# Kernel tuning notes

Hardware: AMD Instinct MI355X
Metric: run time of the kernel (lower is better)

Reference implementation:

```python
import jax, jax.numpy as jnp
import numpy as np

N_LAYERS = 4
D_MODEL = 64        # 8*8 hardcoded in source
D_STATE = 128
D_CONV = 4
EXPAND = 2
HEADDIM = 64        # Mamba2Simple default
D_INNER = EXPAND * D_MODEL            # 128
NHEADS = D_INNER // HEADDIM           # 2
NGROUPS = 1
D_IN_PROJ = 2 * D_INNER + 2 * NGROUPS * D_STATE + NHEADS   # 514
CONV_DIM = D_INNER + 2 * NGROUPS * D_STATE                 # 384
EPS = 1e-5
B_SZ, SEQ = 8, 4096


def setup_inputs() -> dict:
    key = jax.random.key(0)
    ks = jax.random.split(key, 8)
    s = 0.02
    x = jax.random.normal(ks[0], (B_SZ, SEQ, D_MODEL), jnp.float32)
    in_proj_w = jax.random.normal(ks[1], (N_LAYERS, D_IN_PROJ, D_MODEL), jnp.float32) * s
    conv_w = jax.random.normal(ks[2], (N_LAYERS, CONV_DIM, 1, D_CONV), jnp.float32) * 0.2
    conv_b = jnp.zeros((N_LAYERS, CONV_DIM), jnp.float32)
    # dt_bias ~ inverse-softplus of small dt values
    dt_bias = jax.random.uniform(ks[3], (N_LAYERS, NHEADS), jnp.float32, -4.0, 0.0)
    A_log = jnp.log(jax.random.uniform(ks[4], (N_LAYERS, NHEADS), jnp.float32, 1.0, 16.0))
    D = jnp.ones((N_LAYERS, NHEADS), jnp.float32)
    norm_w = jnp.ones((N_LAYERS, D_INNER), jnp.float32)
    out_proj_w = jax.random.normal(ks[5], (N_LAYERS, D_MODEL, D_INNER), jnp.float32) * s
    return {"x": x, "in_proj_w": in_proj_w, "conv_w": conv_w, "conv_b": conv_b,
            "dt_bias": dt_bias, "A_log": A_log, "D": D, "norm_w": norm_w,
            "out_proj_w": out_proj_w}


def _ssm(xh, dt, A, Bm, Cm):
    """Selective-scan SSM. xh:(B,L,H,P) dt:(B,L,H) A:(H,) Bm,Cm:(B,L,S) -> (B,L,H,P)"""
    dA = jnp.exp(dt * A)  # (B,L,H)

    def step(h, inp):
        dA_t, dt_t, x_t, B_t, C_t = inp
        # h: (B,H,P,S)
        h = h * dA_t[:, :, None, None] + (dt_t[:, :, None] * x_t)[..., None] * B_t[:, None, None, :]
        y = jnp.einsum('bhps,bs->bhp', h, C_t)
        return h, y

    b = xh.shape[0]
    h0 = jnp.zeros((b, NHEADS, HEADDIM, D_STATE), xh.dtype)
    xs = (jnp.moveaxis(dA, 1, 0), jnp.moveaxis(dt, 1, 0), jnp.moveaxis(xh, 1, 0),
          jnp.moveaxis(Bm, 1, 0), jnp.moveaxis(Cm, 1, 0))
    _, ys = jax.lax.scan(step, h0, xs)
    return jnp.moveaxis(ys, 0, 1)


def _layer(x, p):
    in_w, cw, cb, dtb, Alog, Dp, nw, ow = p
    zxbcdt = x @ in_w.T                                   # (B,L,514)
    z = zxbcdt[..., :D_INNER]
    xBC = zxbcdt[..., D_INNER:D_INNER + CONV_DIM]
    dt = jax.nn.softplus(zxbcdt[..., -NHEADS:] + dtb)     # (B,L,H)
    # causal depthwise conv over sequence
    xc = jnp.moveaxis(xBC, -1, 1)                         # (B,C,L)
    xc = jax.lax.conv_general_dilated(xc, cw, (1,), [(D_CONV - 1, 0)],
                                      dimension_numbers=('NCH', 'OIH', 'NCH'),
                                      feature_group_count=CONV_DIM)
    xBC = jax.nn.silu(jnp.moveaxis(xc + cb[None, :, None], 1, -1))
    xs = xBC[..., :D_INNER]
    Bm = xBC[..., D_INNER:D_INNER + D_STATE]
    Cm = xBC[..., D_INNER + D_STATE:]
    xh = xs.reshape(xs.shape[0], xs.shape[1], NHEADS, HEADDIM)
    A = -jnp.exp(Alog)                                    # (H,)
    y = _ssm(xh, dt, A, Bm, Cm) + Dp[None, None, :, None] * xh
    y = y.reshape(y.shape[0], y.shape[1], D_INNER)
    # gated RMSNorm (norm_before_gate=False): rmsnorm(y * silu(z)) * w
    y = y * jax.nn.silu(z)
    y = y * jax.lax.rsqrt(jnp.mean(y * y, axis=-1, keepdims=True) + EPS) * nw
    return y @ ow.T


def reference(x, in_proj_w, conv_w, conv_b, dt_bias, A_log, D, norm_w, out_proj_w):
    def body(xc, p):
        return _layer(xc, p) + xc, None
    out, _ = jax.lax.scan(body, x, (in_proj_w, conv_w, conv_b, dt_bias, A_log, D, norm_w, out_proj_w))
    return out
```

## Files before the change

kernel.cpp:

```cpp
#include <hip/hip_runtime.h>
#include <math.h>

#define B_SZ 8
#define SEQ  4096
#define DM   64
#define DI   128
#define NH   2
#define HD   64
#define DS   128
#define DIP  514
#define ZW   512
#define CD   384
#define QC   64
#define NC   64
#define NR   (B_SZ*SEQ)
#define WPAD 576

typedef __attribute__((ext_vector_type(8))) short bf16x8;
typedef __attribute__((ext_vector_type(4))) float f32x4;

__device__ __forceinline__ unsigned short f2bf(float f) {
    union { float f; unsigned int u; } x; x.f = f;
    unsigned int r = x.u + 0x7fffu + ((x.u >> 16) & 1u);
    return (unsigned short)(r >> 16);
}
__device__ __forceinline__ float bf2f(unsigned short h) {
    union { unsigned int u; float f; } x; x.u = ((unsigned int)h) << 16;
    return x.f;
}
__device__ __forceinline__ bf16x8 fragld(const unsigned short* base, int r0, int k0, int ld) {
    int l = threadIdx.x & 63;
    return *(const bf16x8*)(base + (size_t)(r0 + (l & 15)) * ld + k0 + (l >> 4) * 8);
}

__global__ __launch_bounds__(256) void k_wcvt(const float* __restrict__ in_w,
                                              const float* __restrict__ out_w,
                                              unsigned short* __restrict__ Wb,
                                              unsigned short* __restrict__ OWb) {
    int idx = blockIdx.x * 256 + threadIdx.x;
    if (idx < 4 * WPAD * 64) {
        int l = idx / (WPAD * 64), r = idx % (WPAD * 64);
        int n = r >> 6, k = r & 63;
        float v = (n < DIP) ? in_w[(size_t)l * DIP * 64 + (size_t)n * 64 + k] : 0.f;
        Wb[idx] = f2bf(v);
    }
    if (idx < 4 * 64 * 128) OWb[idx] = f2bf(out_w[idx]);
}

__global__ __launch_bounds__(256) void k_xcvt(const float* __restrict__ X,
                                              unsigned short* __restrict__ Xb) {
    int idx = (blockIdx.x * 256 + threadIdx.x) * 4;
    float4 v = *(const float4*)(X + idx);
    uint2 p;
    p.x = f2bf(v.x) | ((unsigned int)f2bf(v.y) << 16);
    p.y = f2bf(v.z) | ((unsigned int)f2bf(v.w) << 16);
    *(uint2*)(Xb + idx) = p;
}

__global__ __launch_bounds__(256) void k_inproj(const unsigned short* __restrict__ Xb,
                                                const unsigned short* __restrict__ Wb,
                                                unsigned short* __restrict__ ZXb,
                                                float* __restrict__ DT) {
    int m0 = blockIdx.x * 256;
    int n0 = blockIdx.y * 64;
    int tid = threadIdx.x;
    int wid = tid >> 6, lane = tid & 63;
    int q4 = lane >> 4, c16 = lane & 15;
    int mb = m0 + wid * 64;
    bf16x8 af[4][2];
#pragma unroll
    for (int mt = 0; mt < 4; mt++)
#pragma unroll
        for (int ks = 0; ks < 2; ks++)
            af[mt][ks] = *(const bf16x8*)(Xb + (size_t)(mb + mt * 16 + c16) * 64 + ks * 32 + q4 * 8);
    if (n0 < 512) {
#pragma unroll
        for (int nt = 0; nt < 4; nt++) {
            bf16x8 bf[2];
#pragma unroll
            for (int ks = 0; ks < 2; ks++)
                bf[ks] = *(const bf16x8*)(Wb + (size_t)(n0 + nt * 16 + c16) * 64 + ks * 32 + q4 * 8);
#pragma unroll
            for (int mt = 0; mt < 4; mt++) {
                f32x4 acc = {0.f, 0.f, 0.f, 0.f};
                acc = __builtin_amdgcn_mfma_f32_16x16x32_bf16(af[mt][0], bf[0], acc, 0, 0, 0);
                acc = __builtin_amdgcn_mfma_f32_16x16x32_bf16(af[mt][1], bf[1], acc, 0, 0, 0);
#pragma unroll
                for (int rr = 0; rr < 4; rr++) {
                    float v = acc[rr];
                    float vn = __shfl_xor(v, 1);
                    if (!(lane & 1)) {
                        unsigned int pk = f2bf(v) | ((unsigned int)f2bf(vn) << 16);
                        *(unsigned int*)(ZXb + (size_t)(mb + mt * 16 + q4 * 4 + rr) * ZW + n0 + nt * 16 + c16) = pk;
                    }
                }
            }
        }
    } else {
        bf16x8 bf[2];
#pragma unroll
        for (int ks = 0; ks < 2; ks++)
            bf[ks] = *(const bf16x8*)(Wb + (size_t)(512 + c16) * 64 + ks * 32 + q4 * 8);
#pragma unroll
        for (int mt = 0; mt < 4; mt++) {
            f32x4 acc = {0.f, 0.f, 0.f, 0.f};
            acc = __builtin_amdgcn_mfma_f32_16x16x32_bf16(af[mt][0], bf[0], acc, 0, 0, 0);
            acc = __builtin_amdgcn_mfma_f32_16x16x32_bf16(af[mt][1], bf[1], acc, 0, 0, 0);
            if (c16 < 2)
#pragma unroll
                for (int rr = 0; rr < 4; rr++)
                    DT[(size_t)(mb + mt * 16 + q4 * 4 + rr) * 2 + c16] = acc[rr];
        }
    }
}

__global__ __launch_bounds__(512, 4) void k_chunk1(
        const unsigned short* __restrict__ ZXb, const float* __restrict__ DT,
        const float* __restrict__ CW, const float* __restrict__ CB,
        const float* __restrict__ dtb, const float* __restrict__ Alog,
        const float* __restrict__ Dv,
        unsigned short* __restrict__ SL, unsigned short* __restrict__ CBuf,
        float* __restrict__ EB,
        float* __restrict__ TB, unsigned short* __restrict__ YBb) {
    __shared__ unsigned short sBt[128][72];
    __shared__ unsigned short sXt[128][72];
    __shared__ unsigned short uBC[2][64][136];
    __shared__ float s_cum[2][64], s_dt[2][64], s_w[2][64];
    unsigned short (*sM)[64][72] = (unsigned short (*)[64][72])&uBC[0][0][0];

    int c = blockIdx.x, b = blockIdx.y;
    size_t rbase = (size_t)b * SEQ + c * QC;
    int tid = threadIdx.x;
    int wid = tid >> 6, lane = tid & 63;

    if (wid < 2) {
        int h = wid, j = lane;
        float raw = DT[(rbase + j) * 2 + h] + dtb[h];
        float dt = (raw > 20.f) ? raw : log1pf(__expf(raw));
        float A = -__expf(Alog[h]);
        float x = dt * A;
        for (int off = 1; off < 64; off <<= 1) {
            float o = __shfl_up(x, off);
            if (lane >= off) x += o;
        }
        float T = __shfl(x, 63);
        s_dt[h][j] = dt;
        s_cum[h][j] = x;
        s_w[h][j] = __expf(T - x) * dt;
        EB[((size_t)(b * NC + c)) * 128 + h * 64 + j] = __expf(x);
        if (j == 0) TB[(b * 2 + h) * NC + c] = __expf(T);
    }
    __syncthreads();

    size_t cbbase = ((size_t)(b * NC + c)) * 8192;
    for (int e = tid; e < 64 * 96; e += 512) {
        int j = e / 96;
        int q = e - j * 96;
        int cc = q * 4;
        int l = c * QC + j;
        const unsigned short* zp = ZXb + (rbase + j) * ZW + 128 + cc;
        uint2 a0 = *(const uint2*)zp;
        uint2 a1 = make_uint2(0, 0), a2 = make_uint2(0, 0), a3 = make_uint2(0, 0);
        if (l >= 1) a1 = *(const uint2*)(zp - ZW);
        if (l >= 2) a2 = *(const uint2*)(zp - 2 * ZW);
        if (l >= 3) a3 = *(const uint2*)(zp - 3 * ZW);
        float v[4];
#pragma unroll
        for (int u = 0; u < 4; u++) {
            unsigned int w0 = (u < 2) ? a0.x : a0.y;
            unsigned int w1 = (u < 2) ? a1.x : a1.y;
            unsigned int w2 = (u < 2) ? a2.x : a2.y;
            unsigned int w3 = (u < 2) ? a3.x : a3.y;
            int sh = (u & 1) * 16;
            float r0 = bf2f((unsigned short)(w0 >> sh));
            float r1 = bf2f((unsigned short)(w1 >> sh));
            float r2 = bf2f((unsigned short)(w2 >> sh));
            float r3 = bf2f((unsigned short)(w3 >> sh));
            float4 wv = *(const float4*)(CW + (cc + u) * 4);
            float t = CB[cc + u] + wv.w * r0 + wv.z * r1 + wv.y * r2 + wv.x * r3;
            v[u] = t / (1.f + __expf(-t));
        }
        if (cc < 128) {
#pragma unroll
            for (int u = 0; u < 4; u++) sXt[cc + u][j] = f2bf(v[u]);
        } else if (cc < 256) {
            int s = cc - 128;
            unsigned int p0 = f2bf(v[0]) | ((unsigned int)f2bf(v[1]) << 16);
            unsigned int p1 = f2bf(v[2]) | ((unsigned int)f2bf(v[3]) << 16);
            *(uint2*)&uBC[0][j][s] = make_uint2(p0, p1);
#pragma unroll
            for (int u = 0; u < 4; u++) sBt[s + u][j] = f2bf(v[u]);
        } else {
            int s = cc - 256;
            unsigned int p0 = f2bf(v[0]) | ((unsigned int)f2bf(v[1]) << 16);
            unsigned int p1 = f2bf(v[2]) | ((unsigned int)f2bf(v[3]) << 16);
            *(uint2*)&uBC[1][j][s] = make_uint2(p0, p1);
            *(uint2*)(CBuf + cbbase + (size_t)j * 128 + s) = make_uint2(p0, p1);
        }
    }
    __syncthreads();

    int q4 = lane >> 4, c16 = lane & 15;
    f32x4 gacc[2];
#pragma unroll
    for (int u = 0; u < 2; u++) {
        int t = wid * 2 + u;
        int it = t >> 2, jt = t & 3;
        f32x4 acc = {0.f, 0.f, 0.f, 0.f};
        for (int ks = 0; ks < 4; ks++) {
            bf16x8 a = fragld(&uBC[1][0][0], it * 16, ks * 32, 136);
            bf16x8 bb = fragld(&uBC[0][0][0], jt * 16, ks * 32, 136);
            acc = __builtin_amdgcn_mfma_f32_16x16x32_bf16(a, bb, acc, 0, 0, 0);
        }
        gacc[u] = acc;
    }
    __syncthreads();
#pragma unroll
    for (int u = 0; u < 2; u++) {
        int t = wid * 2 + u;
        int it = t >> 2, jt = t & 3;
        int j = jt * 16 + c16;
        for (int rr = 0; rr < 4; rr++) {
            int i = it * 16 + q4 * 4 + rr;
            float gv = gacc[u][rr];
            for (int h = 0; h < 2; h++) {
                float m = 0.f;
                if (j <= i) m = gv * __expf(s_cum[h][i] - s_cum[h][j]) * s_dt[h][j];
                sM[h][i][j] = f2bf(m);
            }
        }
    }
    __syncthreads();

#pragma unroll
    for (int u = 0; u < 4; u++) {
        int idx = wid * 4 + u;
        int h = idx >> 4, tt = idx & 15;
        int it = tt >> 2, pt = tt & 3;
        float dco = Dv[h];
        int pg = h * 64 + pt * 16 + c16;
        f32x4 acc;
        for (int rr = 0; rr < 4; rr++) {
            int i = it * 16 + q4 * 4 + rr;
            acc[rr] = dco * bf2f(sXt[pg][i]);
        }
        for (int ks = 0; ks < 2; ks++) {
            bf16x8 a = fragld(&sM[h][0][0], it * 16, ks * 32, 72);
            bf16x8 bb = fragld(&sXt[0][0], h * 64 + pt * 16, ks * 32, 72);
            acc = __builtin_amdgcn_mfma_f32_16x16x32_bf16(a, bb, acc, 0, 0, 0);
        }
        for (int rr = 0; rr < 4; rr++) {
            int i = it * 16 + q4 * 4 + rr;
            float v = acc[rr];
            float vn = __shfl_xor(v, 1);
            if (!(lane & 1)) {
                unsigned int pk = f2bf(v) | ((unsigned int)f2bf(vn) << 16);
                *(unsigned int*)(YBb + (rbase + i) * DI + pg) = pk;
            }
        }
    }
    size_t slbase = ((size_t)(b * NC + c)) * 16384;
#pragma unroll
    for (int u = 0; u < 8; u++) {
        int idx = wid * 8 + u;
        int ptl = idx >> 3, st = idx & 7;
        int h = ptl >> 2;
        f32x4 acc = {0.f, 0.f, 0.f, 0.f};
        for (int ks = 0; ks < 2; ks++) {
            int jb = ks * 32 + (lane >> 4) * 8;
            bf16x8 a = fragld(&sXt[0][0], ptl * 16, ks * 32, 72);
            bf16x8 aw;
#pragma unroll
            for (int t = 0; t < 8; t++) aw[t] = (short)f2bf(bf2f((unsigned short)a[t]) * s_w[h][jb + t]);
            bf16x8 bb = fragld(&sBt[0][0], st * 16, ks * 32, 72);
            acc = __builtin_amdgcn_mfma_f32_16x16x32_bf16(aw, bb, acc, 0, 0, 0);
        }
        int s = st * 16 + c16;
        for (int rr = 0; rr < 4; rr++) {
            int p = ptl * 16 + q4 * 4 + rr;
            float vv = acc[rr];
            float vn = __shfl_xor(vv, 1);
            if (!(lane & 1)) {
                unsigned int pk = f2bf(vv) | ((unsigned int)f2bf(vn) << 16);
                *(unsigned int*)(SL + slbase + (size_t)p * 128 + s) = pk;
            }
        }
    }
}

__global__ __launch_bounds__(256) void k_scan(unsigned short* __restrict__ SL,
                                              const float* __restrict__ TB) {
    int bid = blockIdx.x;
    int b = bid >> 6;
    int ps = (bid & 63) * 256 + threadIdx.x;
    int h = ps >> 13;
    const float* dAp = TB + (b * 2 + h) * NC;
    size_t base = (size_t)(b * NC) * 16384 + ps;
    float hacc = 0.f;
#pragma unroll 8
    for (int cc = 0; cc < NC; cc++) {
        size_t idx = base + (size_t)cc * 16384;
        float slv = bf2f(SL[idx]);
        SL[idx] = f2bf(hacc);
        hacc = hacc * dAp[cc] + slv;
    }
}

__global__ __launch_bounds__(512, 2) void k_fused(
        const unsigned short* __restrict__ SL, const unsigned short* __restrict__ CBuf,
        const float* __restrict__ EB,
        const unsigned short* __restrict__ YBb, const unsigned short* __restrict__ ZXb,
        const float* __restrict__ NW, const unsigned short* __restrict__ OWb,
        unsigned short* __restrict__ Xb, float* __restrict__ OutF, int last) {
    __shared__ __attribute__((aligned(16))) unsigned short sH[128][136];
    __shared__ __attribute__((aligned(16))) unsigned short sE[128][136];
    float* sGf = (float*)&sH[0][0];
    unsigned short (*sG)[136] = (unsigned short (*)[136])&sE[0][0];

    int c = blockIdx.x, b = blockIdx.y;
    size_t rbase = (size_t)b * SEQ + c * QC;
    int tid = threadIdx.x;
    int wid = tid >> 6, lane = tid & 63;
    size_t base = ((size_t)(b * NC + c)) * 16384;
    for (int u = 0; u < 4; u++) {
        int e = u * 512 + tid;
        int row = e >> 4, cb8 = (e & 15) * 8;
        *(uint4*)&sH[row][cb8] = *(const uint4*)(SL + base + (size_t)row * 128 + cb8);
    }
    size_t cbbase = ((size_t)(b * NC + c)) * 8192;
    size_t ebase  = ((size_t)(b * NC + c)) * 128;
    for (int u = 0; u < 2; u++) {
        int idx8 = u * 512 + tid;
        int i = idx8 >> 4, sc = (idx8 & 15) * 8;
        uint4 cv = *(const uint4*)(CBuf + cbbase + (size_t)i * 128 + sc);
        float e0 = EB[ebase + i], e1 = EB[ebase + 64 + i];
        unsigned int w[4] = {cv.x, cv.y, cv.z, cv.w};
        uint4 o0, o1;
        unsigned int* po0 = &o0.x;
        unsigned int* po1 = &o1.x;
#pragma unroll
        for (int t = 0; t < 4; t++) {
            float lo = bf2f((unsigned short)(w[t] & 0xffff));
            float hi = bf2f((unsigned short)(w[t] >> 16));
            po0[t] = f2bf(lo * e0) | ((unsigned int)f2bf(hi * e0) << 16);
            po1[t] = f2bf(lo * e1) | ((unsigned int)f2bf(hi * e1) << 16);
        }
        *(uint4*)&sE[i][sc] = o0;
        *(uint4*)&sE[64 + i][sc] = o1;
    }
    __syncthreads();
    int q4 = lane >> 4, c16 = lane & 15;

    float yv[4][4];
    int tit[4], tpg[4];
#pragma unroll
    for (int u = 0; u < 4; u++) {
        int idx = wid * 4 + u;
        int h = idx >> 4, tt = idx & 15;
        int it = tt >> 2, pt = tt & 3;
        f32x4 acc = {0.f, 0.f, 0.f, 0.f};
        for (int ks = 0; ks < 4; ks++) {
            bf16x8 a = fragld(&sE[0][0], h * 64 + it * 16, ks * 32, 136);
            bf16x8 bb = fragld(&sH[0][0], h * 64 + pt * 16, ks * 32, 136);
            acc = __builtin_amdgcn_mfma_f32_16x16x32_bf16(a, bb, acc, 0, 0, 0);
        }
        int pg = h * 64 + pt * 16 + c16;
        tit[u] = it; tpg[u] = pg;
        for (int rr = 0; rr < 4; rr++) {
            int i = it * 16 + q4 * 4 + rr;
            float y = acc[rr] + bf2f(YBb[(rbase + i) * DI + pg]);
            float z = bf2f(ZXb[(rbase + i) * ZW + pg]);
            yv[u][rr] = y * (z / (1.f + __expf(-z)));
        }
    }
    __syncthreads();
#pragma unroll
    for (int u = 0; u < 4; u++)
        for (int rr = 0; rr < 4; rr++) {
            int i = tit[u] * 16 + q4 * 4 + rr;
            sGf[i * 132 + tpg[u]] = yv[u][rr];
        }
    __syncthreads();
    {
        int row = tid >> 3, p0 = (tid & 7) * 16;
        float g[16];
        float ss = 0.f;
        for (int t2 = 0; t2 < 16; t2++) { g[t2] = sGf[row * 132 + p0 + t2]; ss += g[t2] * g[t2]; }
        ss += __shfl_xor(ss, 1);
        ss += __shfl_xor(ss, 2);
        ss += __shfl_xor(ss, 4);
        float rms = rsqrtf(ss * (1.f / 128.f) + 1e-5f);
        for (int t2 = 0; t2 < 16; t2 += 2) {
            unsigned int pk = f2bf(g[t2] * rms * NW[p0 + t2]) |
                              ((unsigned int)f2bf(g[t2 + 1] * rms * NW[p0 + t2 + 1]) << 16);
            *(unsigned int*)&sG[row][p0 + t2] = pk;
        }
    }
    __syncthreads();
#pragma unroll
    for (int u = 0; u < 2; u++) {
        int t = wid * 2 + u;
        int mt = t >> 2, nt = t & 3;
        f32x4 acc = {0.f, 0.f, 0.f, 0.f};
        for (int ks = 0; ks < 4; ks++) {
            bf16x8 a = fragld(&sG[0][0], mt * 16, ks * 32, 136);
            bf16x8 bb = *(const bf16x8*)(OWb + (size_t)(nt * 16 + c16) * 128 + ks * 32 + q4 * 8);
            acc = __builtin_amdgcn_mfma_f32_16x16x32_bf16(a, bb, acc, 0, 0, 0);
        }
        for (int rr = 0; rr < 4; rr++) {
            int m = mt * 16 + q4 * 4 + rr;
            int n = nt * 16 + c16;
            size_t o = (rbase + m) * DM + n;
            float v = bf2f(Xb[o]) + acc[rr];
            if (last) {
                OutF[o] = v;
            } else {
                float vn = __shfl_xor(v, 1);
                if (!(lane & 1)) {
                    unsigned int pk = f2bf(v) | ((unsigned int)f2bf(vn) << 16);
                    *(unsigned int*)(Xb + o) = pk;
                }
            }
        }
    }
}

extern "C" void kernel_launch(void* const* d_in, const int* in_sizes, int n_in,
                              void* d_out, int out_size, void* d_ws, size_t ws_size,
                              hipStream_t stream) {
    const float* x       = (const float*)d_in[0];
    const float* in_w    = (const float*)d_in[1];
    const float* conv_w  = (const float*)d_in[2];
    const float* conv_b  = (const float*)d_in[3];
    const float* dt_bias = (const float*)d_in[4];
    const float* A_log   = (const float*)d_in[5];
    const float* Dp      = (const float*)d_in[6];
    const float* norm_w  = (const float*)d_in[7];
    const float* out_w   = (const float*)d_in[8];
    float* out = (float*)d_out;
    float* ws  = (float*)d_ws;

    float* dt = ws;
    float* tb = dt + (size_t)NR * 2;
    float* eb = tb + 1024;
    unsigned short* zxb  = (unsigned short*)(eb + (size_t)B_SZ * NC * 128);
    unsigned short* ybb  = zxb + (size_t)NR * ZW;
    unsigned short* sl   = ybb + (size_t)NR * DI;
    unsigned short* cbuf = sl + (size_t)B_SZ * NC * 16384;
    unsigned short* xb   = cbuf + (size_t)B_SZ * NC * 8192;
    unsigned short* wb   = xb + (size_t)NR * DM;
    unsigned short* owb  = wb + (size_t)4 * WPAD * 64;

    k_wcvt<<<(4 * WPAD * 64 + 255) / 256, 256, 0, stream>>>(in_w, out_w, wb, owb);
    k_xcvt<<<NR * DM / 1024, 256, 0, stream>>>(x, xb);

    for (int layer = 0; layer < 4; layer++) {
        k_inproj<<<dim3(NR / 256, 9), 256, 0, stream>>>(xb, wb + (size_t)layer * WPAD * 64, zxb, dt);
        k_chunk1<<<dim3(NC, B_SZ), 512, 0, stream>>>(zxb, dt,
                conv_w + (size_t)layer * CD * 4, conv_b + (size_t)layer * CD,
                dt_bias + layer * NH, A_log + layer * NH, Dp + layer * NH,
                sl, cbuf, eb, tb, ybb);
        k_scan<<<512, 256, 0, stream>>>(sl, tb);
        k_fused<<<dim3(NC, B_SZ), 512, 0, stream>>>(sl, cbuf, eb, ybb, zxb,
                norm_w + layer * DI, owb + (size_t)layer * 64 * 128, xb, out,
                (layer == 3) ? 1 : 0);
    }
}
```

Baseline: 370.3 us.

## Fuse in-projection GEMM into chunk kernel, keep xBC and dt in shared memory

Removes the separate in-projection kernel and computes the projection per chunk inside the chunk kernel, now run with 1024 threads. Only the z part goes to global memory, narrowed to 128 columns. The xBC columns, plus a 3-row halo recomputed from the previous chunk for the causal conv, stay in shared memory, and dt stays in shared memory too. This cuts the global write and read-back of the 512-wide bf16 projection buffer and the dt buffer, and saves one launch per layer. In exchange the halo rows are recomputed, shared memory use grows, and the 1024-thread blocks may lower occupancy.

Result: slower. 414.2 us (+11.9%).

```diff
diff --git a/kernel.cpp b/kernel.cpp
--- a/kernel.cpp
+++ b/kernel.cpp
@@ -9,12 +9,12 @@
 #define HD   64
 #define DS   128
 #define DIP  514
-#define ZW   512
 #define CD   384
 #define QC   64
 #define NC   64
 #define NR   (B_SZ*SEQ)
 #define WPAD 576
+#define ZLD  388
 
 typedef __attribute__((ext_vector_type(8))) short bf16x8;
 typedef __attribute__((ext_vector_type(4))) float f32x4;
@@ -30,7 +30,7 @@
 }
 __device__ __forceinline__ bf16x8 fragld(const unsigned short* base, int r0, int k0, int ld) {
     int l = threadIdx.x & 63;
-    return *(const bf16x8*)(base + (size_t)(r0 + (l & 15)) * ld + k0 + (l >> 4) * 8);
+    return *(const bf16x8*)(base + (ptrdiff_t)(r0 + (l & 15)) * ld + k0 + (l >> 4) * 8);
 }
 
 __global__ __launch_bounds__(256) void k_wcvt(const float* __restrict__ in_w,
@@ -57,85 +57,77 @@
     *(uint2*)(Xb + idx) = p;
 }
 
-__global__ __launch_bounds__(256) void k_inproj(const unsigned short* __restrict__ Xb,
-                                                const unsigned short* __restrict__ Wb,
-                                                unsigned short* __restrict__ ZXb,
-                                                float* __restrict__ DT) {
-    int m0 = blockIdx.x * 256;
-    int n0 = blockIdx.y * 64;
-    int tid = threadIdx.x;
-    int wid = tid >> 6, lane = tid & 63;
-    int q4 = lane >> 4, c16 = lane & 15;
-    int mb = m0 + wid * 64;
-    bf16x8 af[4][2];
-#pragma unroll
-    for (int mt = 0; mt < 4; mt++)
-#pragma unroll
-        for (int ks = 0; ks < 2; ks++)
-            af[mt][ks] = *(const bf16x8*)(Xb + (size_t)(mb + mt * 16 + c16) * 64 + ks * 32 + q4 * 8);
-    if (n0 < 512) {
-#pragma unroll
-        for (int nt = 0; nt < 4; nt++) {
-            bf16x8 bf[2];
-#pragma unroll
-            for (int ks = 0; ks < 2; ks++)
-                bf[ks] = *(const bf16x8*)(Wb + (size_t)(n0 + nt * 16 + c16) * 64 + ks * 32 + q4 * 8);
-#pragma unroll
-            for (int mt = 0; mt < 4; mt++) {
-                f32x4 acc = {0.f, 0.f, 0.f, 0.f};
-                acc = __builtin_amdgcn_mfma_f32_16x16x32_bf16(af[mt][0], bf[0], acc, 0, 0, 0);
-                acc = __builtin_amdgcn_mfma_f32_16x16x32_bf16(af[mt][1], bf[1], acc, 0, 0, 0);
-#pragma unroll
-                for (int rr = 0; rr < 4; rr++) {
-                    float v = acc[rr];
-                    float vn = __shfl_xor(v, 1);
-                    if (!(lane & 1)) {
-                        unsigned int pk = f2bf(v) | ((unsigned int)f2bf(vn) << 16);
-                        *(unsigned int*)(ZXb + (size_t)(mb + mt * 16 + q4 * 4 + rr) * ZW + n0 + nt * 16 + c16) = pk;
-                    }
-                }
-            }
-        }
-    } else {
-        bf16x8 bf[2];
-#pragma unroll
-        for (int ks = 0; ks < 2; ks++)
-            bf[ks] = *(const bf16x8*)(Wb + (size_t)(512 + c16) * 64 + ks * 32 + q4 * 8);
-#pragma unroll
-        for (int mt = 0; mt < 4; mt++) {
-            f32x4 acc = {0.f, 0.f, 0.f, 0.f};
-            acc = __builtin_amdgcn_mfma_f32_16x16x32_bf16(af[mt][0], bf[0], acc, 0, 0, 0);
-            acc = __builtin_amdgcn_mfma_f32_16x16x32_bf16(af[mt][1], bf[1], acc, 0, 0, 0);
-            if (c16 < 2)
-#pragma unroll
-                for (int rr = 0; rr < 4; rr++)
-                    DT[(size_t)(mb + mt * 16 + q4 * 4 + rr) * 2 + c16] = acc[rr];
-        }
-    }
-}
-
-__global__ __launch_bounds__(512, 4) void k_chunk1(
-        const unsigned short* __restrict__ ZXb, const float* __restrict__ DT,
+__global__ __launch_bounds__(1024) void k_mega(
+        const unsigned short* __restrict__ Xb, const unsigned short* __restrict__ Wb,
         const float* __restrict__ CW, const float* __restrict__ CB,
         const float* __restrict__ dtb, const float* __restrict__ Alog,
         const float* __restrict__ Dv,
+        unsigned short* __restrict__ Zb,
         unsigned short* __restrict__ SL, unsigned short* __restrict__ CBuf,
         float* __restrict__ EB,
         float* __restrict__ TB, unsigned short* __restrict__ YBb) {
+    __shared__ unsigned short zrc[68 * ZLD];
     __shared__ unsigned short sBt[128][72];
     __shared__ unsigned short sXt[128][72];
     __shared__ unsigned short uBC[2][64][136];
-    __shared__ float s_cum[2][64], s_dt[2][64], s_w[2][64];
+    __shared__ float s_cum[2][64], s_dt[2][64], s_w[2][64], s_dtraw[2][64];
     unsigned short (*sM)[64][72] = (unsigned short (*)[64][72])&uBC[0][0][0];
 
     int c = blockIdx.x, b = blockIdx.y;
     size_t rbase = (size_t)b * SEQ + c * QC;
     int tid = threadIdx.x;
     int wid = tid >> 6, lane = tid & 63;
+    int q4 = lane >> 4, c16 = lane & 15;
+
+    for (int t = wid; t < 156; t += 16) {
+        int row0, col0, mode, mt, zc0 = 0;
+        if (t < 32) {
+            mt = t >> 3; col0 = (t & 7) * 16; row0 = (int)rbase + mt * 16; mode = 0;
+        } else if (t < 36) {
+            mt = t - 32; col0 = 512; row0 = (int)rbase + mt * 16; mode = 1;
+        } else {
+            int u = t - 36;
+            mt = u / 24; int ntc = u - mt * 24;
+            col0 = 128 + ntc * 16; zc0 = ntc * 16;
+            row0 = (mt < 4) ? (int)rbase + mt * 16 : (int)rbase - 16;
+            if (mt == 4 && c == 0) row0 = (int)rbase;
+            mode = 2;
+        }
+        f32x4 acc = {0.f, 0.f, 0.f, 0.f};
+#pragma unroll
+        for (int ks = 0; ks < 2; ks++) {
+            bf16x8 a = fragld(Xb, row0, ks * 32, 64);
+            bf16x8 bb = fragld(Wb, col0, ks * 32, 64);
+            acc = __builtin_amdgcn_mfma_f32_16x16x32_bf16(a, bb, acc, 0, 0, 0);
+        }
+        if (mode == 0) {
+#pragma unroll
+            for (int rr = 0; rr < 4; rr++) {
+                float v = acc[rr];
+                float vn = __shfl_xor(v, 1);
+                if (!(lane & 1)) {
+                    unsigned int pk = f2bf(v) | ((unsigned int)f2bf(vn) << 16);
+                    *(unsigned int*)(Zb + (size_t)(row0 + q4 * 4 + rr) * DI + col0 + c16) = pk;
+                }
+            }
+        } else if (mode == 1) {
+            if (c16 < 2)
+#pragma unroll
+                for (int rr = 0; rr < 4; rr++)
+                    s_dtraw[c16][mt * 16 + q4 * 4 + rr] = acc[rr];
+        } else {
+#pragma unroll
+            for (int rr = 0; rr < 4; rr++) {
+                int zr = (mt < 4) ? mt * 16 + q4 * 4 + rr + 3 : q4 * 4 + rr - 13;
+                if (zr >= 0) zrc[zr * ZLD + zc0 + c16] = f2bf(acc[rr]);
+            }
+        }
+    }
+    __syncthreads();
 
     if (wid < 2) {
         int h = wid, j = lane;
-        float raw = DT[(rbase + j) * 2 + h] + dtb[h];
+        float raw = s_dtraw[h][j] + dtb[h];
         float dt = (raw > 20.f) ? raw : log1pf(__expf(raw));
         float A = -__expf(Alog[h]);
         float x = dt * A;
@@ -150,20 +142,19 @@
         EB[((size_t)(b * NC + c)) * 128 + h * 64 + j] = __expf(x);
         if (j == 0) TB[(b * 2 + h) * NC + c] = __expf(T);
     }
-    __syncthreads();
 
     size_t cbbase = ((size_t)(b * NC + c)) * 8192;
-    for (int e = tid; e < 64 * 96; e += 512) {
+    for (int e = tid; e < 64 * 96; e += 1024) {
         int j = e / 96;
         int q = e - j * 96;
         int cc = q * 4;
         int l = c * QC + j;
-        const unsigned short* zp = ZXb + (rbase + j) * ZW + 128 + cc;
+        const unsigned short* zp = zrc + (j + 3) * ZLD + cc;
         uint2 a0 = *(const uint2*)zp;
         uint2 a1 = make_uint2(0, 0), a2 = make_uint2(0, 0), a3 = make_uint2(0, 0);
-        if (l >= 1) a1 = *(const uint2*)(zp - ZW);
-        if (l >= 2) a2 = *(const uint2*)(zp - 2 * ZW);
-        if (l >= 3) a3 = *(const uint2*)(zp - 3 * ZW);
+        if (l >= 1) a1 = *(const uint2*)(zp - ZLD);
+        if (l >= 2) a2 = *(const uint2*)(zp - 2 * ZLD);
+        if (l >= 3) a3 = *(const uint2*)(zp - 3 * ZLD);
         float v[4];
 #pragma unroll
         for (int u = 0; u < 4; u++) {
@@ -177,8 +168,8 @@
             float r2 = bf2f((unsigned short)(w2 >> sh));
             float r3 = bf2f((unsigned short)(w3 >> sh));
             float4 wv = *(const float4*)(CW + (cc + u) * 4);
-            float t = CB[cc + u] + wv.w * r0 + wv.z * r1 + wv.y * r2 + wv.x * r3;
-            v[u] = t / (1.f + __expf(-t));
+            float tt = CB[cc + u] + wv.w * r0 + wv.z * r1 + wv.y * r2 + wv.x * r3;
+            v[u] = tt / (1.f + __expf(-tt));
         }
         if (cc < 128) {
 #pragma unroll
@@ -200,29 +191,24 @@
     }
     __syncthreads();
 
-    int q4 = lane >> 4, c16 = lane & 15;
-    f32x4 gacc[2];
-#pragma unroll
-    for (int u = 0; u < 2; u++) {
-        int t = wid * 2 + u;
-        int it = t >> 2, jt = t & 3;
+    f32x4 gacc;
+    {
+        int it = wid >> 2, jt = wid & 3;
         f32x4 acc = {0.f, 0.f, 0.f, 0.f};
         for (int ks = 0; ks < 4; ks++) {
             bf16x8 a = fragld(&uBC[1][0][0], it * 16, ks * 32, 136);
             bf16x8 bb = fragld(&uBC[0][0][0], jt * 16, ks * 32, 136);
             acc = __builtin_amdgcn_mfma_f32_16x16x32_bf16(a, bb, acc, 0, 0, 0);
         }
-        gacc[u] = acc;
-    }
-    __syncthreads();
-#pragma unroll
-    for (int u = 0; u < 2; u++) {
-        int t = wid * 2 + u;
-        int it = t >> 2, jt = t & 3;
+        gacc = acc;
+    }
+    __syncthreads();
+    {
+        int it = wid >> 2, jt = wid & 3;
         int j = jt * 16 + c16;
         for (int rr = 0; rr < 4; rr++) {
             int i = it * 16 + q4 * 4 + rr;
-            float gv = gacc[u][rr];
+            float gv = gacc[rr];
             for (int h = 0; h < 2; h++) {
                 float m = 0.f;
                 if (j <= i) m = gv * __expf(s_cum[h][i] - s_cum[h][j]) * s_dt[h][j];
@@ -233,8 +219,8 @@
     __syncthreads();
 
 #pragma unroll
-    for (int u = 0; u < 4; u++) {
-        int idx = wid * 4 + u;
+    for (int u = 0; u < 2; u++) {
+        int idx = wid * 2 + u;
         int h = idx >> 4, tt = idx & 15;
         int it = tt >> 2, pt = tt & 3;
         float dco = Dv[h];
@@ -261,8 +247,8 @@
     }
     size_t slbase = ((size_t)(b * NC + c)) * 16384;
 #pragma unroll
-    for (int u = 0; u < 8; u++) {
-        int idx = wid * 8 + u;
+    for (int u = 0; u < 4; u++) {
+        int idx = wid * 4 + u;
         int ptl = idx >> 3, st = idx & 7;
         int h = ptl >> 2;
         f32x4 acc = {0.f, 0.f, 0.f, 0.f};
@@ -309,7 +295,7 @@
 __global__ __launch_bounds__(512, 2) void k_fused(
         const unsigned short* __restrict__ SL, const unsigned short* __restrict__ CBuf,
         const float* __restrict__ EB,
-        const unsigned short* __restrict__ YBb, const unsigned short* __restrict__ ZXb,
+        const unsigned short* __restrict__ YBb, const unsigned short* __restrict__ Zb,
         const float* __restrict__ NW, const unsigned short* __restrict__ OWb,
         unsigned short* __restrict__ Xb, float* __restrict__ OutF, int last) {
     __shared__ __attribute__((aligned(16))) unsigned short sH[128][136];
@@ -369,7 +355,7 @@
         for (int rr = 0; rr < 4; rr++) {
             int i = it * 16 + q4 * 4 + rr;
             float y = acc[rr] + bf2f(YBb[(rbase + i) * DI + pg]);
-            float z = bf2f(ZXb[(rbase + i) * ZW + pg]);
+            float z = bf2f(Zb[(rbase + i) * DI + pg]);
             yv[u][rr] = y * (z / (1.f + __expf(-z)));
         }
     }
@@ -440,11 +426,10 @@
     float* out = (float*)d_out;
     float* ws  = (float*)d_ws;
 
-    float* dt = ws;
-    float* tb = dt + (size_t)NR * 2;
+    float* tb = ws;
     float* eb = tb + 1024;
-    unsigned short* zxb  = (unsigned short*)(eb + (size_t)B_SZ * NC * 128);
-    unsigned short* ybb  = zxb + (size_t)NR * ZW;
+    unsigned short* zb   = (unsigned short*)(eb + (size_t)B_SZ * NC * 128);
+    unsigned short* ybb  = zb + (size_t)NR * DI;
     unsigned short* sl   = ybb + (size_t)NR * DI;
     unsigned short* cbuf = sl + (size_t)B_SZ * NC * 16384;
     unsigned short* xb   = cbuf + (size_t)B_SZ * NC * 8192;
@@ -455,13 +440,12 @@
     k_xcvt<<<NR * DM / 1024, 256, 0, stream>>>(x, xb);
 
     for (int layer = 0; layer < 4; layer++) {
-        k_inproj<<<dim3(NR / 256, 9), 256, 0, stream>>>(xb, wb + (size_t)layer * WPAD * 64, zxb, dt);
-        k_chunk1<<<dim3(NC, B_SZ), 512, 0, stream>>>(zxb, dt,
+        k_mega<<<dim3(NC, B_SZ), 1024, 0, stream>>>(xb, wb + (size_t)layer * WPAD * 64,
                 conv_w + (size_t)layer * CD * 4, conv_b + (size_t)layer * CD,
                 dt_bias + layer * NH, A_log + layer * NH, Dp + layer * NH,
-                sl, cbuf, eb, tb, ybb);
+                zb, sl, cbuf, eb, tb, ybb);
         k_scan<<<512, 256, 0, stream>>>(sl, tb);
-        k_fused<<<dim3(NC, B_SZ), 512, 0, stream>>>(sl, cbuf, eb, ybb, zxb,
+        k_fused<<<dim3(NC, B_SZ), 512, 0, stream>>>(sl, cbuf, eb, ybb, zb,
                 norm_w + layer * DI, owb + (size_t)layer * 64 * 128, xb, out,
                 (layer == 3) ? 1 : 0);
     }
```

## Double block size of chunk and fused kernels, vectorize inter-chunk scan

Applied to the files above, without the earlier changes.

k_chunk1 and k_fused now launch 1024 threads per block, so each wave handles half as many MFMA tiles and load iterations. One redundant barrier after the dt prefix computation is removed. k_scan now has each thread process four packed bf16 states per chunk, prefetching the next chunk's values, and launches with fewer threads. The tighter launch bounds (1024, 8) may force a low register budget and cause spills, and the scan now runs with less thread-level parallelism.

Result: slower. 389.1 us (+5.1%).

```diff
diff --git a/kernel.cpp b/kernel.cpp
--- a/kernel.cpp
+++ b/kernel.cpp
@@ -30,7 +30,7 @@
 }
 __device__ __forceinline__ bf16x8 fragld(const unsigned short* base, int r0, int k0, int ld) {
     int l = threadIdx.x & 63;
-    return *(const bf16x8*)(base + (size_t)(r0 + (l & 15)) * ld + k0 + (l >> 4) * 8);
+    return *(const bf16x8*)(base + (ptrdiff_t)(r0 + (l & 15)) * ld + k0 + (l >> 4) * 8);
 }
 
 __global__ __launch_bounds__(256) void k_wcvt(const float* __restrict__ in_w,
@@ -114,7 +114,7 @@
     }
 }
 
-__global__ __launch_bounds__(512, 4) void k_chunk1(
+__global__ __launch_bounds__(1024, 8) void k_chunk1(
         const unsigned short* __restrict__ ZXb, const float* __restrict__ DT,
         const float* __restrict__ CW, const float* __restrict__ CB,
         const float* __restrict__ dtb, const float* __restrict__ Alog,
@@ -132,6 +132,7 @@
     size_t rbase = (size_t)b * SEQ + c * QC;
     int tid = threadIdx.x;
     int wid = tid >> 6, lane = tid & 63;
+    int q4 = lane >> 4, c16 = lane & 15;
 
     if (wid < 2) {
         int h = wid, j = lane;
@@ -150,10 +151,9 @@
         EB[((size_t)(b * NC + c)) * 128 + h * 64 + j] = __expf(x);
         if (j == 0) TB[(b * 2 + h) * NC + c] = __expf(T);
     }
-    __syncthreads();
 
     size_t cbbase = ((size_t)(b * NC + c)) * 8192;
-    for (int e = tid; e < 64 * 96; e += 512) {
+    for (int e = tid; e < 64 * 96; e += 1024) {
         int j = e / 96;
         int q = e - j * 96;
         int cc = q * 4;
@@ -177,8 +177,8 @@
             float r2 = bf2f((unsigned short)(w2 >> sh));
             float r3 = bf2f((unsigned short)(w3 >> sh));
             float4 wv = *(const float4*)(CW + (cc + u) * 4);
-            float t = CB[cc + u] + wv.w * r0 + wv.z * r1 + wv.y * r2 + wv.x * r3;
-            v[u] = t / (1.f + __expf(-t));
+            float tt = CB[cc + u] + wv.w * r0 + wv.z * r1 + wv.y * r2 + wv.x * r3;
+            v[u] = tt / (1.f + __expf(-tt));
         }
         if (cc < 128) {
 #pragma unroll
@@ -200,29 +200,24 @@
     }
     __syncthreads();
 
-    int q4 = lane >> 4, c16 = lane & 15;
-    f32x4 gacc[2];
-#pragma unroll
-    for (int u = 0; u < 2; u++) {
-        int t = wid * 2 + u;
-        int it = t >> 2, jt = t & 3;
+    f32x4 gacc;
+    {
+        int it = wid >> 2, jt = wid & 3;
         f32x4 acc = {0.f, 0.f, 0.f, 0.f};
         for (int ks = 0; ks < 4; ks++) {
             bf16x8 a = fragld(&uBC[1][0][0], it * 16, ks * 32, 136);
             bf16x8 bb = fragld(&uBC[0][0][0], jt * 16, ks * 32, 136);
             acc = __builtin_amdgcn_mfma_f32_16x16x32_bf16(a, bb, acc, 0, 0, 0);
         }
-        gacc[u] = acc;
-    }
-    __syncthreads();
-#pragma unroll
-    for (int u = 0; u < 2; u++) {
-        int t = wid * 2 + u;
-        int it = t >> 2, jt = t & 3;
+        gacc = acc;
+    }
+    __syncthreads();
+    {
+        int it = wid >> 2, jt = wid & 3;
         int j = jt * 16 + c16;
         for (int rr = 0; rr < 4; rr++) {
             int i = it * 16 + q4 * 4 + rr;
-            float gv = gacc[u][rr];
+            float gv = gacc[rr];
             for (int h = 0; h < 2; h++) {
                 float m = 0.f;
                 if (j <= i) m = gv * __expf(s_cum[h][i] - s_cum[h][j]) * s_dt[h][j];
@@ -233,8 +228,8 @@
     __syncthreads();
 
 #pragma unroll
-    for (int u = 0; u < 4; u++) {
-        int idx = wid * 4 + u;
+    for (int u = 0; u < 2; u++) {
+        int idx = wid * 2 + u;
         int h = idx >> 4, tt = idx & 15;
         int it = tt >> 2, pt = tt & 3;
         float dco = Dv[h];
@@ -261,8 +256,8 @@
     }
     size_t slbase = ((size_t)(b * NC + c)) * 16384;
 #pragma unroll
-    for (int u = 0; u < 8; u++) {
-        int idx = wid * 8 + u;
+    for (int u = 0; u < 4; u++) {
+        int idx = wid * 4 + u;
         int ptl = idx >> 3, st = idx & 7;
         int h = ptl >> 2;
         f32x4 acc = {0.f, 0.f, 0.f, 0.f};
@@ -288,25 +283,37 @@
     }
 }
 
-__global__ __launch_bounds__(256) void k_scan(unsigned short* __restrict__ SL,
+__global__ __launch_bounds__(128) void k_scan(unsigned short* __restrict__ SL,
                                               const float* __restrict__ TB) {
     int bid = blockIdx.x;
-    int b = bid >> 6;
-    int ps = (bid & 63) * 256 + threadIdx.x;
+    int b = bid >> 5;
+    int ps = ((bid & 31) * 128 + threadIdx.x) * 4;
     int h = ps >> 13;
     const float* dAp = TB + (b * 2 + h) * NC;
     size_t base = (size_t)(b * NC) * 16384 + ps;
-    float hacc = 0.f;
-#pragma unroll 8
+    float h0 = 0.f, h1 = 0.f, h2 = 0.f, h3 = 0.f;
+    uint2 cur = *(const uint2*)(SL + base);
     for (int cc = 0; cc < NC; cc++) {
-        size_t idx = base + (size_t)cc * 16384;
-        float slv = bf2f(SL[idx]);
-        SL[idx] = f2bf(hacc);
-        hacc = hacc * dAp[cc] + slv;
-    }
-}
-
-__global__ __launch_bounds__(512, 2) void k_fused(
+        uint2 nxt = make_uint2(0, 0);
+        if (cc + 1 < NC) nxt = *(const uint2*)(SL + base + (size_t)(cc + 1) * 16384);
+        float dA = dAp[cc];
+        float s0 = bf2f((unsigned short)(cur.x & 0xffff));
+        float s1 = bf2f((unsigned short)(cur.x >> 16));
+        float s2 = bf2f((unsigned short)(cur.y & 0xffff));
+        float s3 = bf2f((unsigned short)(cur.y >> 16));
+        uint2 st;
+        st.x = f2bf(h0) | ((unsigned int)f2bf(h1) << 16);
+        st.y = f2bf(h2) | ((unsigned int)f2bf(h3) << 16);
+        *(uint2*)(SL + base + (size_t)cc * 16384) = st;
+        h0 = h0 * dA + s0;
+        h1 = h1 * dA + s1;
+        h2 = h2 * dA + s2;
+        h3 = h3 * dA + s3;
+        cur = nxt;
+    }
+}
+
+__global__ __launch_bounds__(1024, 8) void k_fused(
         const unsigned short* __restrict__ SL, const unsigned short* __restrict__ CBuf,
         const float* __restrict__ EB,
         const unsigned short* __restrict__ YBb, const unsigned short* __restrict__ ZXb,
@@ -322,16 +329,15 @@
     int tid = threadIdx.x;
     int wid = tid >> 6, lane = tid & 63;
     size_t base = ((size_t)(b * NC + c)) * 16384;
-    for (int u = 0; u < 4; u++) {
-        int e = u * 512 + tid;
+    for (int u = 0; u < 2; u++) {
+        int e = u * 1024 + tid;
         int row = e >> 4, cb8 = (e & 15) * 8;
         *(uint4*)&sH[row][cb8] = *(const uint4*)(SL + base + (size_t)row * 128 + cb8);
     }
     size_t cbbase = ((size_t)(b * NC + c)) * 8192;
     size_t ebase  = ((size_t)(b * NC + c)) * 128;
-    for (int u = 0; u < 2; u++) {
-        int idx8 = u * 512 + tid;
-        int i = idx8 >> 4, sc = (idx8 & 15) * 8;
+    {
+        int i = tid >> 4, sc = (tid & 15) * 8;
         uint4 cv = *(const uint4*)(CBuf + cbbase + (size_t)i * 128 + sc);
         float e0 = EB[ebase + i], e1 = EB[ebase + 64 + i];
         unsigned int w[4] = {cv.x, cv.y, cv.z, cv.w};
@@ -351,11 +357,11 @@
     __syncthreads();
     int q4 = lane >> 4, c16 = lane & 15;
 
-    float yv[4][4];
-    int tit[4], tpg[4];
-#pragma unroll
-    for (int u = 0; u < 4; u++) {
-        int idx = wid * 4 + u;
+    float yv[2][4];
+    int tit[2], tpg[2];
+#pragma unroll
+    for (int u = 0; u < 2; u++) {
+        int idx = wid * 2 + u;
         int h = idx >> 4, tt = idx & 15;
         int it = tt >> 2, pt = tt & 3;
         f32x4 acc = {0.f, 0.f, 0.f, 0.f};
@@ -375,32 +381,32 @@
     }
     __syncthreads();
 #pragma unroll
-    for (int u = 0; u < 4; u++)
+    for (int u = 0; u < 2; u++)
         for (int rr = 0; rr < 4; rr++) {
             int i = tit[u] * 16 + q4 * 4 + rr;
             sGf[i * 132 + tpg[u]] = yv[u][rr];
         }
     __syncthreads();
     {
-        int row = tid >> 3, p0 = (tid & 7) * 16;
-        float g[16];
+        int row = tid >> 4, part = tid & 15;
+        int d0 = part * 8;
+        float g[8];
         float ss = 0.f;
-        for (int t2 = 0; t2 < 16; t2++) { g[t2] = sGf[row * 132 + p0 + t2]; ss += g[t2] * g[t2]; }
+        for (int t2 = 0; t2 < 8; t2++) { g[t2] = sGf[row * 132 + d0 + t2]; ss += g[t2] * g[t2]; }
         ss += __shfl_xor(ss, 1);
         ss += __shfl_xor(ss, 2);
         ss += __shfl_xor(ss, 4);
+        ss += __shfl_xor(ss, 8);
         float rms = rsqrtf(ss * (1.f / 128.f) + 1e-5f);
-        for (int t2 = 0; t2 < 16; t2 += 2) {
-            unsigned int pk = f2bf(g[t2] * rms * NW[p0 + t2]) |
-                              ((unsigned int)f2bf(g[t2 + 1] * rms * NW[p0 + t2 + 1]) << 16);
-            *(unsigned int*)&sG[row][p0 + t2] = pk;
-        }
-    }
-    __syncthreads();
-#pragma unroll
-    for (int u = 0; u < 2; u++) {
-        int t = wid * 2 + u;
-        int mt = t >> 2, nt = t & 3;
+        for (int t2 = 0; t2 < 8; t2 += 2) {
+            unsigned int pk = f2bf(g[t2] * rms * NW[d0 + t2]) |
+                              ((unsigned int)f2bf(g[t2 + 1] * rms * NW[d0 + t2 + 1]) << 16);
+            *(unsigned int*)&sG[row][d0 + t2] = pk;
+        }
+    }
+    __syncthreads();
+    {
+        int mt = wid >> 2, nt = wid & 3;
         f32x4 acc = {0.f, 0.f, 0.f, 0.f};
         for (int ks = 0; ks < 4; ks++) {
             bf16x8 a = fragld(&sG[0][0], mt * 16, ks * 32, 136);
@@ -456,13 +462,13 @@
 
     for (int layer = 0; layer < 4; layer++) {
         k_inproj<<<dim3(NR / 256, 9), 256, 0, stream>>>(xb, wb + (size_t)layer * WPAD * 64, zxb, dt);
-        k_chunk1<<<dim3(NC, B_SZ), 512, 0, stream>>>(zxb, dt,
+        k_chunk1<<<dim3(NC, B_SZ), 1024, 0, stream>>>(zxb, dt,
                 conv_w + (size_t)layer * CD * 4, conv_b + (size_t)layer * CD,
                 dt_bias + layer * NH, A_log + layer * NH, Dp + layer * NH,
                 sl, cbuf, eb, tb, ybb);
-        k_scan<<<512, 256, 0, stream>>>(sl, tb);
-        k_fused<<<dim3(NC, B_SZ), 512, 0, stream>>>(sl, cbuf, eb, ybb, zxb,
-                norm_w + layer * DI, owb + (size_t)layer * 64 * 128, xb, out,
+        k_scan<<<256, 128, 0, stream>>>(sl, tb);
+        k_fused<<<dim3(NC, B_SZ), 1024, 0, stream>>>(sl, cbuf, eb, ybb,
+                zxb, norm_w + layer * DI, owb + (size_t)layer * 64 * 128, xb, out,
                 (layer == 3) ? 1 : 0);
     }
 }
```
